# Kernel tuning notes

Hardware: AMD Instinct MI355X
Metric: run time of the kernel (lower is better)

## Reference

```python
import jax, jax.numpy as jnp
import numpy as np

D_MODEL = 1024
N_HEADS = 16
HEAD_DIM = D_MODEL // N_HEADS
ROPE_BASE = 10000.0


def _rope_cos_sin(t, dtype):
    # inv_freq over half the head dim, standard RoPE (GPT-NeoX style)
    inv_freq = 1.0 / (ROPE_BASE ** (jnp.arange(0, HEAD_DIM, 2, dtype=jnp.float32) / HEAD_DIM))
    freqs = jnp.arange(t, dtype=jnp.float32)[:, None] * inv_freq[None, :]  # [t, hd/2]
    emb = jnp.concatenate([freqs, freqs], axis=-1)  # [t, hd]
    return jnp.cos(emb).astype(dtype), jnp.sin(emb).astype(dtype)


def _rotate_half(x):
    x1, x2 = jnp.split(x, 2, axis=-1)
    return jnp.concatenate([-x2, x1], axis=-1)


def _apply_rope(x, cos, sin):
    # x: [b, h, t, hd]; cos/sin: [t, hd]
    return x * cos[None, None] + _rotate_half(x) * sin[None, None]


def setup_inputs() -> dict:
    key = jax.random.key(0)
    kx, kqkv, kout = jax.random.split(key, 3)
    x = jax.random.normal(kx, (4, 2048, D_MODEL), dtype=jnp.float32)
    scale = 1.0 / np.sqrt(D_MODEL)
    Wqkv = jax.random.normal(kqkv, (D_MODEL, 3 * D_MODEL), dtype=jnp.float32) * scale
    Wout = jax.random.normal(kout, (D_MODEL, D_MODEL), dtype=jnp.float32) * scale
    return {"x": x, "Wqkv": Wqkv, "Wout": Wout}


def reference(x, Wqkv, Wout):
    b, t, _ = x.shape
    qkv = (x @ Wqkv).reshape(b, t, 3, N_HEADS, HEAD_DIM)
    q, k, v = qkv[:, :, 0], qkv[:, :, 1], qkv[:, :, 2]  # [b, t, h, hd]
    q = q.transpose(0, 2, 1, 3)  # [b, h, t, hd]
    k = k.transpose(0, 2, 1, 3)
    v = v.transpose(0, 2, 1, 3)
    cos, sin = _rope_cos_sin(t, x.dtype)
    q = _apply_rope(q, cos, sin)
    k = _apply_rope(k, cos, sin)
    # causal SDPA
    scores = jnp.einsum("bhqd,bhkd->bhqk", q, k) / np.sqrt(HEAD_DIM)
    causal = jnp.tril(jnp.ones((t, t), dtype=bool))
    scores = jnp.where(causal[None, None], scores, jnp.finfo(scores.dtype).min)
    attn = jax.nn.softmax(scores, axis=-1)
    out = jnp.einsum("bhqk,bhkd->bhqd", attn, v)
    out = out.transpose(0, 2, 1, 3).reshape(b, t, D_MODEL)
    return out @ Wout
```

## Files before the change

### kernel.cpp

```cpp
#include <hip/hip_runtime.h>
#include <cstdint>
#include <cstddef>

typedef __bf16 bf16;
typedef __bf16 bf16x8 __attribute__((ext_vector_type(8)));
typedef __bf16 bf16x4 __attribute__((ext_vector_type(4)));
typedef float  f32x4  __attribute__((ext_vector_type(4)));

#define MFMA16(a, b, c) __builtin_amdgcn_mfma_f32_16x16x32_bf16((a), (b), (c), 0, 0, 0)

static constexpr int BB   = 4;
static constexpr int TT   = 2048;
static constexpr int DM   = 1024;
static constexpr int NH   = 16;
static constexpr int HD   = 64;
static constexpr int TOK  = BB * TT;
static constexpr int NQKV = 3 * DM;

__device__ inline void gload16(const void* g, void* l) {
    __builtin_amdgcn_global_load_lds((const __attribute__((address_space(1))) void*)g,
                                     (__attribute__((address_space(3))) void*)l, 16, 0, 0);
}

__device__ inline int swz(int x) { return x ^ ((x >> 3) & 0x70); }

__global__ void k_cvt(const float* __restrict__ in, bf16* __restrict__ out, int n) {
    int i = (blockIdx.x * blockDim.x + threadIdx.x) * 4;
    if (i >= n) return;
    float4 v = *(const float4*)(in + i);
    bf16x4 o;
    o[0] = (bf16)v.x; o[1] = (bf16)v.y; o[2] = (bf16)v.z; o[3] = (bf16)v.w;
    *(bf16x4*)(out + i) = o;
}

__global__ void k_transpose_cvt(const float* __restrict__ in, bf16* __restrict__ out,
                                int R, int C) {
    __shared__ bf16 tl[64 * 72];
    int tid = threadIdx.x;
    int c0 = blockIdx.x * 64, r0 = blockIdx.y * 64;
#pragma unroll
    for (int rep = 0; rep < 4; rep++) {
        int r = rep * 16 + (tid >> 4);
        int c = (tid & 15) * 4;
        float4 v = *(const float4*)(in + (size_t)(r0 + r) * C + c0 + c);
        tl[r * 72 + c + 0] = (bf16)v.x;
        tl[r * 72 + c + 1] = (bf16)v.y;
        tl[r * 72 + c + 2] = (bf16)v.z;
        tl[r * 72 + c + 3] = (bf16)v.w;
    }
    __syncthreads();
#pragma unroll
    for (int rep = 0; rep < 4; rep++) {
        int cc = rep * 16 + (tid >> 4);
        int rr = (tid & 15) * 4;
        bf16x4 o;
        o[0] = tl[(rr + 0) * 72 + cc];
        o[1] = tl[(rr + 1) * 72 + cc];
        o[2] = tl[(rr + 2) * 72 + cc];
        o[3] = tl[(rr + 3) * 72 + cc];
        *(bf16x4*)(out + (size_t)(c0 + cc) * R + r0 + rr) = o;
    }
}

__global__ void k_rope_tab(float* __restrict__ ct, float* __restrict__ st) {
    int i = blockIdx.x * blockDim.x + threadIdx.x;
    int t = i >> 5, j = i & 31;
    float invf = powf(10000.0f, -(float)j * (1.0f / 32.0f));
    float a = (float)t * invf;
    ct[i] = cosf(a);
    st[i] = sinf(a);
}

template <int MODE>
__global__ __launch_bounds__(256) void k_gemm_bt(
    const bf16* __restrict__ A, const bf16* __restrict__ Bt,
    int M, int N, int K,
    float* __restrict__ outF,
    bf16* __restrict__ qbuf, bf16* __restrict__ kbuf, bf16* __restrict__ vbuf,
    const float* __restrict__ ct, const float* __restrict__ st, float qscale) {
    __shared__ bf16 lA[128 * 64];
    __shared__ bf16 lB[128 * 64];
    int tid = threadIdx.x;
    int l = tid & 63, wid = tid >> 6;
    int wm = wid >> 1, wn = wid & 1;
    int bn = blockIdx.x, bm = blockIdx.y;
    const bf16* Ab = A + (size_t)bm * 128 * K;
    const bf16* Bb = Bt + (size_t)bn * 128 * K;
    int srow = l >> 3, scol = (l & 7) * 8;
    f32x4 acc[4][4] = {};
    for (int kt = 0; kt < K; kt += 64) {
        __syncthreads();
#pragma unroll
        for (int i = 0; i < 4; i++) {
            int chunk = wid * 4 + i;
            gload16(Ab + (size_t)(chunk * 8 + srow) * K + kt + scol, &lA[chunk * 512]);
            gload16(Bb + (size_t)(chunk * 8 + srow) * K + kt + scol, &lB[chunk * 512]);
        }
        __syncthreads();
#pragma unroll
        for (int kk = 0; kk < 2; kk++) {
            bf16x8 af[4], bfr[4];
#pragma unroll
            for (int mi = 0; mi < 4; mi++)
                af[mi] = *(const bf16x8*)&lA[(wm * 64 + mi * 16 + (l & 15)) * 64 + kk * 32 + (l >> 4) * 8];
#pragma unroll
            for (int ni = 0; ni < 4; ni++)
                bfr[ni] = *(const bf16x8*)&lB[(wn * 64 + ni * 16 + (l & 15)) * 64 + kk * 32 + (l >> 4) * 8];
#pragma unroll
            for (int mi = 0; mi < 4; mi++)
#pragma unroll
                for (int ni = 0; ni < 4; ni++)
                    acc[mi][ni] = MFMA16(af[mi], bfr[ni], acc[mi][ni]);
        }
    }
    if (MODE == 2) {
#pragma unroll
        for (int mi = 0; mi < 4; mi++) {
            int m0 = bm * 128 + wm * 64 + mi * 16 + ((l >> 4) << 2);
#pragma unroll
            for (int ni = 0; ni < 4; ni++) {
                int n = bn * 128 + wn * 64 + ni * 16 + (l & 15);
#pragma unroll
                for (int rj = 0; rj < 4; rj++)
                    outF[(size_t)(m0 + rj) * N + n] = acc[mi][ni][rj];
            }
        }
    } else {
        int n0 = bn * 128 + wn * 64;
        int sQ = n0 >> 10;
        int h = (n0 & 1023) >> 6;
        if (sQ == 2) {
#pragma unroll
            for (int ni = 0; ni < 4; ni++) {
                int d = ni * 16 + (l & 15);
#pragma unroll
                for (int mi = 0; mi < 4; mi++) {
                    int m0 = bm * 128 + wm * 64 + mi * 16 + ((l >> 4) << 2);
                    int b = m0 >> 11, t0 = m0 & 2047;
                    bf16x4 pv;
#pragma unroll
                    for (int rj = 0; rj < 4; rj++) pv[rj] = (bf16)acc[mi][ni][rj];
                    *(bf16x4*)(vbuf + ((size_t)((b * NH + h) * HD + d)) * TT + t0) = pv;
                }
            }
        } else {
            float qs = (sQ == 0) ? qscale : 1.0f;
            bf16* obuf = (sQ == 0) ? qbuf : kbuf;
#pragma unroll
            for (int mi = 0; mi < 4; mi++) {
                int m0 = bm * 128 + wm * 64 + mi * 16 + ((l >> 4) << 2);
                int b = m0 >> 11, t0 = m0 & 2047;
#pragma unroll
                for (int rj = 0; rj < 4; rj++) {
                    int t = t0 + rj;
                    bf16* dst = obuf + ((size_t)(b * NH + h) * TT + t) * HD;
                    const float* crow = ct + t * 32;
                    const float* srow = st + t * 32;
#pragma unroll
                    for (int ni2 = 0; ni2 < 2; ni2++) {
                        int d = ni2 * 16 + (l & 15);
                        float cs = crow[d], sn = srow[d];
                        float a  = acc[mi][ni2][rj];
                        float b2 = acc[mi][ni2 + 2][rj];
                        dst[d]      = (bf16)(qs * (a  * cs - b2 * sn));
                        dst[d + 32] = (bf16)(qs * (b2 * cs + a  * sn));
                    }
                }
            }
        }
    }
}

__global__ __launch_bounds__(256, 3) void k_attn(
    const bf16* __restrict__ Q, const bf16* __restrict__ K,
    const bf16* __restrict__ Vt, bf16* __restrict__ O) {
    __shared__ bf16 lK[2][4096];
    __shared__ bf16 lV[2][4096];
    __shared__ bf16 lP[64 * 72];
    int tid = threadIdx.x;
    int l = tid & 63, w = tid >> 6;
    int flat = blockIdx.x + (blockIdx.y << 4);
    int xcd = flat & 7, rank = flat >> 3;
    int bh = xcd * 8 + (rank >> 4);
    int p = rank & 15;
    const char* KbB = (const char*)(K + (size_t)bh * TT * HD);
    const char* VbB = (const char*)(Vt + (size_t)bh * HD * TT);
    int b = bh >> 4, h = bh & 15;

    bf16x8 ones;
#pragma unroll
    for (int e = 0; e < 8; e++) ones[e] = (bf16)1.0f;

#define STAGE(nb, j) do {                                                                  \
    int X0_ = w * 1024 + l * 16;                                                           \
    const char* Kj_ = KbB + (size_t)(j) * 8192;                                            \
    gload16(Kj_ + swz(X0_),        (char*)lK[nb] + w * 1024);                              \
    gload16(Kj_ + swz(X0_ + 4096), (char*)lK[nb] + w * 1024 + 4096);                       \
    int o0_ = swz(X0_), o1_ = swz(X0_ + 4096);                                             \
    gload16(VbB + (size_t)(o0_ >> 7) * (TT * 2) + (size_t)(j) * 128 + (o0_ & 127),         \
            (char*)lV[nb] + w * 1024);                                                     \
    gload16(VbB + (size_t)(o1_ >> 7) * (TT * 2) + (size_t)(j) * 128 + (o1_ & 127),         \
            (char*)lV[nb] + w * 1024 + 4096);                                              \
} while (0)

    for (int half = 0; half < 2; half++) {
        int s = (half == 0) ? (31 - p) : p;
        int r0 = s * 64;
        int nblk = s + 1;
        const bf16* Qb = Q + ((size_t)bh * TT + r0 + w * 16) * HD;
        bf16x8 qa[2];
#pragma unroll
        for (int kk = 0; kk < 2; kk++)
            qa[kk] = *(const bf16x8*)(Qb + (size_t)(l & 15) * HD + kk * 32 + (l >> 4) * 8);

        f32x4 oacc[4] = {};
        f32x4 lacc = {};

        STAGE(0, 0);
        __syncthreads();
        int cur = 0;
        for (int j = 0; j < nblk; j++) {
            if (j + 1 < nblk) STAGE(cur ^ 1, j + 1);
            f32x4 sc[4] = {};
#pragma unroll
            for (int kk = 0; kk < 2; kk++)
#pragma unroll
                for (int nj = 0; nj < 4; nj++) {
                    int rr = nj * 16 + (l & 15);
                    int L = rr * 128 + (kk * 32 + (l >> 4) * 8) * 2;
                    bf16x8 kb = *(const bf16x8*)((const char*)lK[cur] + (L ^ ((rr & 7) << 4)));
                    sc[nj] = MFMA16(qa[kk], kb, sc[nj]);
                }
            if (j == nblk - 1) {
                int row0 = r0 + w * 16 + ((l >> 4) << 2);
#pragma unroll
                for (int nj = 0; nj < 4; nj++) {
                    int col = j * 64 + nj * 16 + (l & 15);
#pragma unroll
                    for (int rj = 0; rj < 4; rj++)
                        if (col > row0 + rj) sc[nj][rj] = -1e30f;
                }
            }
            {
                int pr0 = w * 16 + ((l >> 4) << 2);
#pragma unroll
                for (int nj = 0; nj < 4; nj++) {
                    int pc = nj * 16 + (l & 15);
#pragma unroll
                    for (int rj = 0; rj < 4; rj++)
                        lP[(pr0 + rj) * 72 + pc] = (bf16)exp2f(sc[nj][rj] - 16.0f);
                }
            }
#pragma unroll
            for (int kk = 0; kk < 2; kk++) {
                bf16x8 pa = *(const bf16x8*)&lP[(w * 16 + (l & 15)) * 72 + kk * 32 + (l >> 4) * 8];
                lacc = MFMA16(pa, ones, lacc);
#pragma unroll
                for (int nd = 0; nd < 4; nd++) {
                    int dd = nd * 16 + (l & 15);
                    int L = dd * 128 + (kk * 32 + (l >> 4) * 8) * 2;
                    bf16x8 vbf = *(const bf16x8*)((const char*)lV[cur] + (L ^ ((dd & 7) << 4)));
                    oacc[nd] = MFMA16(pa, vbf, oacc[nd]);
                }
            }
            __syncthreads();
            cur ^= 1;
        }
#pragma unroll
        for (int rj = 0; rj < 4; rj++) {
            int t = r0 + w * 16 + ((l >> 4) << 2) + rj;
            float inv = 1.0f / lacc[rj];
            size_t base = ((size_t)b * TT + t) * DM + h * HD;
#pragma unroll
            for (int nd = 0; nd < 4; nd++)
                O[base + nd * 16 + (l & 15)] = (bf16)(oacc[nd][rj] * inv);
        }
    }
#undef STAGE
}

extern "C" void kernel_launch(void* const* d_in, const int* in_sizes, int n_in,
                              void* d_out, int out_size, void* d_ws, size_t ws_size,
                              hipStream_t stream) {
    const float* x    = (const float*)d_in[0];
    const float* Wqkv = (const float*)d_in[1];
    const float* Wout = (const float*)d_in[2];
    float* out = (float*)d_out;

    char* ws = (char*)d_ws;
    size_t off = 0;
    auto alloc = [&](size_t bytes) {
        void* p = ws + off;
        off += (bytes + 255) & ~(size_t)255;
        return p;
    };
    bf16* xb    = (bf16*)alloc((size_t)TOK * DM * 2);
    bf16* wqkvt = (bf16*)alloc((size_t)NQKV * DM * 2);
    bf16* woutt = (bf16*)alloc((size_t)DM * DM * 2);
    bf16* qr    = (bf16*)alloc((size_t)TOK * DM * 2);
    bf16* kr    = (bf16*)alloc((size_t)TOK * DM * 2);
    bf16* vt    = (bf16*)alloc((size_t)TOK * DM * 2);
    bf16* ob    = (bf16*)alloc((size_t)TOK * DM * 2);
    float* ct   = (float*)alloc((size_t)TT * 32 * 4);
    float* st   = (float*)alloc((size_t)TT * 32 * 4);
    (void)ws_size; (void)in_sizes; (void)n_in; (void)out_size;

    k_cvt<<<TOK * DM / 4 / 256, 256, 0, stream>>>(x, xb, TOK * DM);
    k_transpose_cvt<<<dim3(NQKV / 64, DM / 64), 256, 0, stream>>>(Wqkv, wqkvt, DM, NQKV);
    k_transpose_cvt<<<dim3(DM / 64, DM / 64), 256, 0, stream>>>(Wout, woutt, DM, DM);
    k_rope_tab<<<TT * 32 / 256, 256, 0, stream>>>(ct, st);
    k_gemm_bt<1><<<dim3(NQKV / 128, TOK / 128), 256, 0, stream>>>(
        xb, wqkvt, TOK, NQKV, DM, nullptr, qr, kr, vt,
        ct, st, 0.125f * 1.4426950408889634f);
    k_attn<<<dim3(16, BB * NH), 256, 0, stream>>>(qr, kr, vt, ob);
    k_gemm_bt<2><<<dim3(DM / 128, TOK / 128), 256, 0, stream>>>(
        ob, woutt, TOK, DM, DM, out, nullptr, nullptr, nullptr,
        nullptr, nullptr, 0.0f);
}
```

Baseline: 221.5 us.

## Software-pipeline attention: overlap QK of next block with PV of previous

Restructures the attention kernel so each iteration computes QK^T for block j while doing PV for block j-1, using a double-buffered P tile and separate K/V staging. The aim is to hide exp/LDS latency behind MFMA work, with s_setprio raising priority around the MFMA section. The grid also moves from 16 to 32 blocks per head, one query tile each, ordered longest first, instead of pairing tiles in a two-half loop. The -16 softmax offset is folded into the accumulator initial value. This costs more LDS and a less balanced per-block workload.

```diff
diff --git a/kernel.cpp b/kernel.cpp
--- a/kernel.cpp
+++ b/kernel.cpp
@@ -176,13 +176,13 @@
     const bf16* __restrict__ Vt, bf16* __restrict__ O) {
     __shared__ bf16 lK[2][4096];
     __shared__ bf16 lV[2][4096];
-    __shared__ bf16 lP[64 * 72];
+    __shared__ bf16 lP[2][64 * 72];
     int tid = threadIdx.x;
     int l = tid & 63, w = tid >> 6;
-    int flat = blockIdx.x + (blockIdx.y << 4);
+    int flat = blockIdx.x + (blockIdx.y << 5);
     int xcd = flat & 7, rank = flat >> 3;
-    int bh = xcd * 8 + (rank >> 4);
-    int p = rank & 15;
+    int bh = xcd * 8 + (rank >> 5);
+    int s = 31 - (rank & 31);
     const char* KbB = (const char*)(K + (size_t)bh * TT * HD);
     const char* VbB = (const char*)(Vt + (size_t)bh * HD * TT);
     int b = bh >> 4, h = bh & 15;
@@ -191,11 +191,15 @@
 #pragma unroll
     for (int e = 0; e < 8; e++) ones[e] = (bf16)1.0f;
 
-#define STAGE(nb, j) do {                                                                  \
+#define STAGE_K(nb, j) do {                                                                \
     int X0_ = w * 1024 + l * 16;                                                           \
     const char* Kj_ = KbB + (size_t)(j) * 8192;                                            \
     gload16(Kj_ + swz(X0_),        (char*)lK[nb] + w * 1024);                              \
     gload16(Kj_ + swz(X0_ + 4096), (char*)lK[nb] + w * 1024 + 4096);                       \
+} while (0)
+
+#define STAGE_V(nb, j) do {                                                                \
+    int X0_ = w * 1024 + l * 16;                                                           \
     int o0_ = swz(X0_), o1_ = swz(X0_ + 4096);                                             \
     gload16(VbB + (size_t)(o0_ >> 7) * (TT * 2) + (size_t)(j) * 128 + (o0_ & 127),         \
             (char*)lV[nb] + w * 1024);                                                     \
@@ -203,80 +207,104 @@
             (char*)lV[nb] + w * 1024 + 4096);                                              \
 } while (0)
 
-    for (int half = 0; half < 2; half++) {
-        int s = (half == 0) ? (31 - p) : p;
-        int r0 = s * 64;
-        int nblk = s + 1;
-        const bf16* Qb = Q + ((size_t)bh * TT + r0 + w * 16) * HD;
-        bf16x8 qa[2];
-#pragma unroll
-        for (int kk = 0; kk < 2; kk++)
-            qa[kk] = *(const bf16x8*)(Qb + (size_t)(l & 15) * HD + kk * 32 + (l >> 4) * 8);
-
-        f32x4 oacc[4] = {};
-        f32x4 lacc = {};
-
-        STAGE(0, 0);
+#define QKJ(kbuf) do {                                                                     \
+    _Pragma("unroll") for (int kk = 0; kk < 2; kk++)                                       \
+    _Pragma("unroll") for (int nj = 0; nj < 4; nj++) {                                     \
+        int rr = nj * 16 + (l & 15);                                                       \
+        int L = rr * 128 + (kk * 32 + (l >> 4) * 8) * 2;                                   \
+        bf16x8 kbv = *(const bf16x8*)((const char*)lK[kbuf] + (L ^ ((rr & 7) << 4)));      \
+        sc[nj] = MFMA16(qa[kk], kbv, sc[nj]);                                              \
+    }                                                                                      \
+} while (0)
+
+#define PVJ(vbuf, pbuf) do {                                                               \
+    _Pragma("unroll") for (int kk = 0; kk < 2; kk++) {                                     \
+        bf16x8 pa = *(const bf16x8*)&lP[pbuf][(w * 16 + (l & 15)) * 72 + kk * 32 + (l >> 4) * 8]; \
+        lacc = MFMA16(pa, ones, lacc);                                                     \
+        _Pragma("unroll") for (int nd = 0; nd < 4; nd++) {                                 \
+            int dd = nd * 16 + (l & 15);                                                   \
+            int L = dd * 128 + (kk * 32 + (l >> 4) * 8) * 2;                               \
+            bf16x8 vbf = *(const bf16x8*)((const char*)lV[vbuf] + (L ^ ((dd & 7) << 4)));  \
+            oacc[nd] = MFMA16(pa, vbf, oacc[nd]);                                          \
+        }                                                                                  \
+    }                                                                                      \
+} while (0)
+
+#define EXPW(pbuf, jj) do {                                                                \
+    if ((jj) == nblk - 1) {                                                                \
+        int row0_ = r0 + w * 16 + ((l >> 4) << 2);                                         \
+        _Pragma("unroll") for (int nj = 0; nj < 4; nj++) {                                 \
+            int col_ = (jj) * 64 + nj * 16 + (l & 15);                                     \
+            _Pragma("unroll") for (int rj = 0; rj < 4; rj++)                               \
+                if (col_ > row0_ + rj) sc[nj][rj] = -1e30f;                                \
+        }                                                                                  \
+    }                                                                                      \
+    int pr0_ = w * 16 + ((l >> 4) << 2);                                                   \
+    _Pragma("unroll") for (int nj = 0; nj < 4; nj++) {                                     \
+        int pc_ = nj * 16 + (l & 15);                                                      \
+        _Pragma("unroll") for (int rj = 0; rj < 4; rj++)                                   \
+            lP[pbuf][(pr0_ + rj) * 72 + pc_] = (bf16)exp2f(sc[nj][rj]);                    \
+    }                                                                                      \
+} while (0)
+
+    int r0 = s * 64;
+    int nblk = s + 1;
+    const bf16* Qb = Q + ((size_t)bh * TT + r0 + w * 16) * HD;
+    bf16x8 qa[2];
+#pragma unroll
+    for (int kk = 0; kk < 2; kk++)
+        qa[kk] = *(const bf16x8*)(Qb + (size_t)(l & 15) * HD + kk * 32 + (l >> 4) * 8);
+
+    f32x4 oacc[4] = {};
+    f32x4 lacc = {};
+
+    STAGE_K(0, 0);
+    __syncthreads();
+    {
+        if (nblk > 1) STAGE_K(1, 1);
+        STAGE_V(0, 0);
+        f32x4 sc[4];
+#pragma unroll
+        for (int nj = 0; nj < 4; nj++)
+#pragma unroll
+            for (int rj = 0; rj < 4; rj++) sc[nj][rj] = -16.0f;
+        __builtin_amdgcn_s_setprio(1);
+        QKJ(0);
+        __builtin_amdgcn_s_setprio(0);
+        EXPW(0, 0);
         __syncthreads();
-        int cur = 0;
-        for (int j = 0; j < nblk; j++) {
-            if (j + 1 < nblk) STAGE(cur ^ 1, j + 1);
-            f32x4 sc[4] = {};
-#pragma unroll
-            for (int kk = 0; kk < 2; kk++)
-#pragma unroll
-                for (int nj = 0; nj < 4; nj++) {
-                    int rr = nj * 16 + (l & 15);
-                    int L = rr * 128 + (kk * 32 + (l >> 4) * 8) * 2;
-                    bf16x8 kb = *(const bf16x8*)((const char*)lK[cur] + (L ^ ((rr & 7) << 4)));
-                    sc[nj] = MFMA16(qa[kk], kb, sc[nj]);
-                }
-            if (j == nblk - 1) {
-                int row0 = r0 + w * 16 + ((l >> 4) << 2);
-#pragma unroll
-                for (int nj = 0; nj < 4; nj++) {
-                    int col = j * 64 + nj * 16 + (l & 15);
-#pragma unroll
-                    for (int rj = 0; rj < 4; rj++)
-                        if (col > row0 + rj) sc[nj][rj] = -1e30f;
-                }
-            }
-            {
-                int pr0 = w * 16 + ((l >> 4) << 2);
-#pragma unroll
-                for (int nj = 0; nj < 4; nj++) {
-                    int pc = nj * 16 + (l & 15);
-#pragma unroll
-                    for (int rj = 0; rj < 4; rj++)
-                        lP[(pr0 + rj) * 72 + pc] = (bf16)exp2f(sc[nj][rj] - 16.0f);
-                }
-            }
-#pragma unroll
-            for (int kk = 0; kk < 2; kk++) {
-                bf16x8 pa = *(const bf16x8*)&lP[(w * 16 + (l & 15)) * 72 + kk * 32 + (l >> 4) * 8];
-                lacc = MFMA16(pa, ones, lacc);
-#pragma unroll
-                for (int nd = 0; nd < 4; nd++) {
-                    int dd = nd * 16 + (l & 15);
-                    int L = dd * 128 + (kk * 32 + (l >> 4) * 8) * 2;
-                    bf16x8 vbf = *(const bf16x8*)((const char*)lV[cur] + (L ^ ((dd & 7) << 4)));
-                    oacc[nd] = MFMA16(pa, vbf, oacc[nd]);
-                }
-            }
-            __syncthreads();
-            cur ^= 1;
-        }
-#pragma unroll
-        for (int rj = 0; rj < 4; rj++) {
-            int t = r0 + w * 16 + ((l >> 4) << 2) + rj;
-            float inv = 1.0f / lacc[rj];
-            size_t base = ((size_t)b * TT + t) * DM + h * HD;
-#pragma unroll
-            for (int nd = 0; nd < 4; nd++)
-                O[base + nd * 16 + (l & 15)] = (bf16)(oacc[nd][rj] * inv);
-        }
-    }
-#undef STAGE
+    }
+    for (int j = 1; j < nblk; j++) {
+        if (j + 1 < nblk) STAGE_K((j + 1) & 1, j + 1);
+        STAGE_V(j & 1, j);
+        f32x4 sc[4];
+#pragma unroll
+        for (int nj = 0; nj < 4; nj++)
+#pragma unroll
+            for (int rj = 0; rj < 4; rj++) sc[nj][rj] = -16.0f;
+        __builtin_amdgcn_s_setprio(1);
+        QKJ(j & 1);
+        PVJ((j - 1) & 1, (j - 1) & 1);
+        __builtin_amdgcn_s_setprio(0);
+        EXPW(j & 1, j);
+        __syncthreads();
+    }
+    PVJ((nblk - 1) & 1, (nblk - 1) & 1);
+
+#pragma unroll
+    for (int rj = 0; rj < 4; rj++) {
+        int t = r0 + w * 16 + ((l >> 4) << 2) + rj;
+        float inv = 1.0f / lacc[rj];
+        size_t base = ((size_t)b * TT + t) * DM + h * HD;
+#pragma unroll
+        for (int nd = 0; nd < 4; nd++)
+            O[base + nd * 16 + (l & 15)] = (bf16)(oacc[nd][rj] * inv);
+    }
+#undef STAGE_K
+#undef STAGE_V
+#undef QKJ
+#undef PVJ
+#undef EXPW
 }
 
 extern "C" void kernel_launch(void* const* d_in, const int* in_sizes, int n_in,
@@ -312,7 +340,7 @@
     k_gemm_bt<1><<<dim3(NQKV / 128, TOK / 128), 256, 0, stream>>>(
         xb, wqkvt, TOK, NQKV, DM, nullptr, qr, kr, vt,
         ct, st, 0.125f * 1.4426950408889634f);
-    k_attn<<<dim3(16, BB * NH), 256, 0, stream>>>(qr, kr, vt, ob);
+    k_attn<<<dim3(32, BB * NH), 256, 0, stream>>>(qr, kr, vt, ob);
     k_gemm_bt<2><<<dim3(DM / 128, TOK / 128), 256, 0, stream>>>(
         ob, woutt, TOK, DM, DM, out, nullptr, nullptr, nullptr,
         nullptr, nullptr, 0.0f);
```

New measurement: 221.8 us. About the same (+0.1%).

## Restructure attention to 128-row query tiles with 32x32 MFMA and direct V loads

Applied to the files above, without the earlier changes.

The attention kernel now processes 128 query rows per block, each wave owning 32 rows, and uses 32x32x16 MFMA instead of 16x16x32. V is no longer staged through LDS and is read straight from global memory into registers each block. The -16 softmax offset is folded into the score accumulator's initial value, per-wave causal skipping is added, s_setprio hints wrap the MFMA bursts, and occupancy is raised to 4 blocks per CU. The goal is fewer LDS operations and a smaller LDS footprint, at the cost of uncoalesced, latency-exposed global V loads and larger register pressure.

```diff
diff --git a/kernel.cpp b/kernel.cpp
--- a/kernel.cpp
+++ b/kernel.cpp
@@ -6,8 +6,10 @@
 typedef __bf16 bf16x8 __attribute__((ext_vector_type(8)));
 typedef __bf16 bf16x4 __attribute__((ext_vector_type(4)));
 typedef float  f32x4  __attribute__((ext_vector_type(4)));
+typedef float  f32x16 __attribute__((ext_vector_type(16)));
 
 #define MFMA16(a, b, c) __builtin_amdgcn_mfma_f32_16x16x32_bf16((a), (b), (c), 0, 0, 0)
+#define MFMA32(a, b, c) __builtin_amdgcn_mfma_f32_32x32x16_bf16((a), (b), (c), 0, 0, 0)
 
 static constexpr int BB   = 4;
 static constexpr int TT   = 2048;
@@ -171,12 +173,11 @@
     }
 }
 
-__global__ __launch_bounds__(256, 3) void k_attn(
+__global__ __launch_bounds__(256, 4) void k_attn(
     const bf16* __restrict__ Q, const bf16* __restrict__ K,
     const bf16* __restrict__ Vt, bf16* __restrict__ O) {
     __shared__ bf16 lK[2][4096];
-    __shared__ bf16 lV[2][4096];
-    __shared__ bf16 lP[64 * 72];
+    __shared__ bf16 lP[128 * 68];
     int tid = threadIdx.x;
     int l = tid & 63, w = tid >> 6;
     int flat = blockIdx.x + (blockIdx.y << 4);
@@ -184,99 +185,108 @@
     int bh = xcd * 8 + (rank >> 4);
     int p = rank & 15;
     const char* KbB = (const char*)(K + (size_t)bh * TT * HD);
-    const char* VbB = (const char*)(Vt + (size_t)bh * HD * TT);
+    const bf16* Vb = Vt + (size_t)bh * HD * TT;
     int b = bh >> 4, h = bh & 15;
 
     bf16x8 ones;
 #pragma unroll
     for (int e = 0; e < 8; e++) ones[e] = (bf16)1.0f;
 
-#define STAGE(nb, j) do {                                                                  \
+#define STAGE_K(nb, j) do {                                                                \
     int X0_ = w * 1024 + l * 16;                                                           \
     const char* Kj_ = KbB + (size_t)(j) * 8192;                                            \
     gload16(Kj_ + swz(X0_),        (char*)lK[nb] + w * 1024);                              \
     gload16(Kj_ + swz(X0_ + 4096), (char*)lK[nb] + w * 1024 + 4096);                       \
-    int o0_ = swz(X0_), o1_ = swz(X0_ + 4096);                                             \
-    gload16(VbB + (size_t)(o0_ >> 7) * (TT * 2) + (size_t)(j) * 128 + (o0_ & 127),         \
-            (char*)lV[nb] + w * 1024);                                                     \
-    gload16(VbB + (size_t)(o1_ >> 7) * (TT * 2) + (size_t)(j) * 128 + (o1_ & 127),         \
-            (char*)lV[nb] + w * 1024 + 4096);                                              \
 } while (0)
 
     for (int half = 0; half < 2; half++) {
-        int s = (half == 0) ? (31 - p) : p;
-        int r0 = s * 64;
-        int nblk = s + 1;
-        const bf16* Qb = Q + ((size_t)bh * TT + r0 + w * 16) * HD;
-        bf16x8 qa[2];
-#pragma unroll
-        for (int kk = 0; kk < 2; kk++)
-            qa[kk] = *(const bf16x8*)(Qb + (size_t)(l & 15) * HD + kk * 32 + (l >> 4) * 8);
-
-        f32x4 oacc[4] = {};
-        f32x4 lacc = {};
-
-        STAGE(0, 0);
+        int s = (half == 0) ? (15 - p) : p;
+        int r0 = s * 128;
+        int nblk = 2 * s + 2;
+        int wrow = r0 + w * 32;
+        const bf16* Qb = Q + ((size_t)bh * TT + wrow) * HD;
+        bf16x8 qa[4];
+#pragma unroll
+        for (int kc = 0; kc < 4; kc++)
+            qa[kc] = *(const bf16x8*)(Qb + (size_t)(l & 31) * HD + kc * 16 + (l >> 5) * 8);
+
+        f32x16 oacc[2] = {};
+        f32x16 lacc = {};
+
+        STAGE_K(0, 0);
         __syncthreads();
         int cur = 0;
         for (int j = 0; j < nblk; j++) {
-            if (j + 1 < nblk) STAGE(cur ^ 1, j + 1);
-            f32x4 sc[4] = {};
-#pragma unroll
-            for (int kk = 0; kk < 2; kk++)
-#pragma unroll
-                for (int nj = 0; nj < 4; nj++) {
-                    int rr = nj * 16 + (l & 15);
-                    int L = rr * 128 + (kk * 32 + (l >> 4) * 8) * 2;
-                    bf16x8 kb = *(const bf16x8*)((const char*)lK[cur] + (L ^ ((rr & 7) << 4)));
-                    sc[nj] = MFMA16(qa[kk], kb, sc[nj]);
-                }
-            if (j == nblk - 1) {
-                int row0 = r0 + w * 16 + ((l >> 4) << 2);
-#pragma unroll
-                for (int nj = 0; nj < 4; nj++) {
-                    int col = j * 64 + nj * 16 + (l & 15);
-#pragma unroll
-                    for (int rj = 0; rj < 4; rj++)
-                        if (col > row0 + rj) sc[nj][rj] = -1e30f;
-                }
-            }
-            {
-                int pr0 = w * 16 + ((l >> 4) << 2);
-#pragma unroll
-                for (int nj = 0; nj < 4; nj++) {
-                    int pc = nj * 16 + (l & 15);
-#pragma unroll
-                    for (int rj = 0; rj < 4; rj++)
-                        lP[(pr0 + rj) * 72 + pc] = (bf16)exp2f(sc[nj][rj] - 16.0f);
-                }
-            }
-#pragma unroll
-            for (int kk = 0; kk < 2; kk++) {
-                bf16x8 pa = *(const bf16x8*)&lP[(w * 16 + (l & 15)) * 72 + kk * 32 + (l >> 4) * 8];
-                lacc = MFMA16(pa, ones, lacc);
-#pragma unroll
-                for (int nd = 0; nd < 4; nd++) {
-                    int dd = nd * 16 + (l & 15);
-                    int L = dd * 128 + (kk * 32 + (l >> 4) * 8) * 2;
-                    bf16x8 vbf = *(const bf16x8*)((const char*)lV[cur] + (L ^ ((dd & 7) << 4)));
-                    oacc[nd] = MFMA16(pa, vbf, oacc[nd]);
-                }
+            if (j + 1 < nblk) STAGE_K(cur ^ 1, j + 1);
+            if (j * 64 <= wrow + 31) {
+                f32x16 sc[2];
+#pragma unroll
+                for (int r = 0; r < 16; r++) { sc[0][r] = -16.0f; sc[1][r] = -16.0f; }
+                __builtin_amdgcn_s_setprio(1);
+#pragma unroll
+                for (int kc = 0; kc < 4; kc++)
+#pragma unroll
+                    for (int nj = 0; nj < 2; nj++) {
+                        int rr = nj * 32 + (l & 31);
+                        int L = rr * 128 + (kc * 16 + (l >> 5) * 8) * 2;
+                        bf16x8 kb = *(const bf16x8*)((const char*)lK[cur] + (L ^ ((rr & 7) << 4)));
+                        sc[nj] = MFMA32(qa[kc], kb, sc[nj]);
+                    }
+                __builtin_amdgcn_s_setprio(0);
+                if (j * 64 + 63 > wrow) {
+#pragma unroll
+                    for (int nj = 0; nj < 2; nj++) {
+                        int colg = j * 64 + nj * 32 + (l & 31);
+#pragma unroll
+                        for (int r = 0; r < 16; r++) {
+                            int rowq = wrow + (r & 3) + 8 * (r >> 2) + 4 * (l >> 5);
+                            if (colg > rowq) sc[nj][r] = -1e30f;
+                        }
+                    }
+                }
+                {
+                    int prB = w * 32 + 4 * (l >> 5);
+#pragma unroll
+                    for (int nj = 0; nj < 2; nj++) {
+                        int pc = nj * 32 + (l & 31);
+#pragma unroll
+                        for (int r = 0; r < 16; r++)
+                            lP[(prB + (r & 3) + 8 * (r >> 2)) * 68 + pc] = (bf16)exp2f(sc[nj][r]);
+                    }
+                }
+                bf16x8 vb[4][2];
+#pragma unroll
+                for (int kc = 0; kc < 4; kc++)
+#pragma unroll
+                    for (int dt = 0; dt < 2; dt++)
+                        vb[kc][dt] = *(const bf16x8*)(Vb + (size_t)(dt * 32 + (l & 31)) * TT
+                                                      + j * 64 + kc * 16 + (l >> 5) * 8);
+                __builtin_amdgcn_s_setprio(1);
+#pragma unroll
+                for (int kc = 0; kc < 4; kc++) {
+                    bf16x8 pa = *(const bf16x8*)&lP[(w * 32 + (l & 31)) * 68 + kc * 16 + (l >> 5) * 8];
+                    lacc = MFMA32(pa, ones, lacc);
+#pragma unroll
+                    for (int dt = 0; dt < 2; dt++)
+                        oacc[dt] = MFMA32(pa, vb[kc][dt], oacc[dt]);
+                }
+                __builtin_amdgcn_s_setprio(0);
             }
             __syncthreads();
             cur ^= 1;
         }
 #pragma unroll
-        for (int rj = 0; rj < 4; rj++) {
-            int t = r0 + w * 16 + ((l >> 4) << 2) + rj;
-            float inv = 1.0f / lacc[rj];
+        for (int r = 0; r < 16; r++) {
+            int rq = (r & 3) + 8 * (r >> 2) + 4 * (l >> 5);
+            int t = wrow + rq;
+            float inv = 1.0f / lacc[r];
             size_t base = ((size_t)b * TT + t) * DM + h * HD;
 #pragma unroll
-            for (int nd = 0; nd < 4; nd++)
-                O[base + nd * 16 + (l & 15)] = (bf16)(oacc[nd][rj] * inv);
-        }
-    }
-#undef STAGE
+            for (int dt = 0; dt < 2; dt++)
+                O[base + dt * 32 + (l & 31)] = (bf16)(oacc[dt][r] * inv);
+        }
+    }
+#undef STAGE_K
 }
 
 extern "C" void kernel_launch(void* const* d_in, const int* in_sizes, int n_in,
```

Result: slower. 369.3 us (+66.7%).
